# Kernel optimization log

Measured on AMD Instinct MI355X. Metric: run time of the kernel, lower is better.

Reference implementation:

```python
import jax, jax.numpy as jnp
import numpy as np
import math

NB_STEPS = 50  # matches init kwarg nb_steps


def cc_quadrature(nb_steps):
    # Clenshaw-Curtis weights/nodes, identical to UMNN's compute_cc_weights.
    lam = np.arange(nb_steps + 1, dtype=np.float64).reshape(-1, 1)
    lam = np.cos((lam @ lam.T) * math.pi / nb_steps)
    lam[:, 0] = 0.5
    lam[:, -1] = 0.5 * lam[:, -1]
    lam = lam * 2.0 / nb_steps
    W = np.arange(nb_steps + 1, dtype=np.float64).reshape(-1, 1)
    W[np.arange(1, nb_steps + 1, 2)] = 0
    W = 2.0 / (1.0 - W ** 2)
    W[0] = 1
    W[np.arange(1, nb_steps + 1, 2)] = 0
    cc_weights = (lam.T @ W).astype(np.float32)                 # [K, 1]
    steps = np.cos(np.arange(nb_steps + 1, dtype=np.float64).reshape(-1, 1)
                   * math.pi / nb_steps).astype(np.float32)     # [K, 1]
    return jnp.asarray(cc_weights), jnp.asarray(steps)


def integrand_mlp(xh, W1, b1, W2, b2, W3, b3, W4, b4):
    y = jax.nn.relu(jnp.einsum('bkd,hd->bkh', xh, W1) + b1)
    y = jax.nn.relu(jnp.einsum('bkh,gh->bkg', y, W2) + b2)
    y = jax.nn.relu(jnp.einsum('bkg,fg->bkf', y, W3) + b3)
    y = jnp.einsum('bkf,of->bko', y, W4) + b4
    return jax.nn.elu(y) + 1.0


def setup_inputs() -> dict:
    key = jax.random.key(0)
    ks = jax.random.split(key, 10)
    B, HD, IN_D = 16384, 128, 64
    x = jax.random.normal(ks[0], (B, 1), dtype=jnp.float32)
    h = jax.random.normal(ks[1], (B, IN_D - 1), dtype=jnp.float32)
    def lin(k, fan_out, fan_in):
        return jax.random.normal(k, (fan_out, fan_in), dtype=jnp.float32) / np.sqrt(fan_in)
    return {
        'x': x, 'h': h,
        'W1': lin(ks[2], HD, IN_D), 'b1': jax.random.normal(ks[3], (HD,), dtype=jnp.float32) * 0.01,
        'W2': lin(ks[4], HD, HD),   'b2': jax.random.normal(ks[5], (HD,), dtype=jnp.float32) * 0.01,
        'W3': lin(ks[6], HD, HD),   'b3': jax.random.normal(ks[7], (HD,), dtype=jnp.float32) * 0.01,
        'W4': lin(ks[8], 1, HD),    'b4': jax.random.normal(ks[9], (1,), dtype=jnp.float32) * 0.01,
    }


def reference(x, h, W1, b1, W2, b2, W3, b3, W4, b4):
    cc_w, steps = cc_quadrature(NB_STEPS)          # [K,1], [K,1]
    xmax = jnp.max(x) + 10.0
    x0 = x                                          # [B,1]
    xT = jnp.zeros_like(x) + xmax                   # xfinal broadcast
    # quadrature points X_steps: [B, K, 1]
    X = x0[:, None, :] + (xT - x0)[:, None, :] * (steps[None, :, :] + 1.0) * 0.5
    B, K = X.shape[0], X.shape[1]
    hK = jnp.broadcast_to(h[:, None, :], (B, K, h.shape[1]))
    xh = jnp.concatenate([X, hK], axis=-1)          # [B, K, in_d]
    f = integrand_mlp(xh, W1, b1, W2, b2, W3, b3, W4, b4)  # [B, K, 1]
    z = jnp.sum(f * cc_w[None, :, :], axis=1)       # [B, 1]
    return z * (xT - x0) * 0.5
```

## Files before the change

kernel.cpp:

```cpp
#include <hip/hip_runtime.h>
#include <hip/hip_bf16.h>
#include <math.h>


#define B_N    16384
#define KQ     51
#define HD     128
#define IND    64
#define BLK    128
#define RPB    16
#define GRID   (B_N / RPB)
#define TPB    ((RPB * KQ) / 16)

typedef __attribute__((ext_vector_type(8))) short short8;
typedef __attribute__((ext_vector_type(4))) float f32x4;

union S8U { short8 s8; unsigned u[4]; };

__device__ __forceinline__ unsigned short f2bf(float f) {
    __hip_bfloat16 t = __float2bfloat16(f);
    return *reinterpret_cast<unsigned short*>(&t);
}

#if defined(__gfx950__) && defined(__has_builtin)
#if __has_builtin(__builtin_amdgcn_cvt_pk_bf16_f32)
#define HAVE_PK_BF16 1
#endif
#endif

__device__ __forceinline__ unsigned pk_bf16(float lo, float hi) {
#ifdef HAVE_PK_BF16
    typedef __attribute__((ext_vector_type(2))) __bf16 bfv2;
    bfv2 r = __builtin_amdgcn_cvt_pk_bf16_f32(lo, hi);
    return *reinterpret_cast<unsigned*>(&r);
#else
    return (unsigned)f2bf(lo) | ((unsigned)f2bf(hi) << 16);
#endif
}

__launch_bounds__(BLK, 2)
__global__ void umnn_fused(const float* __restrict__ x,  const float* __restrict__ h,
                           const float* __restrict__ W1, const float* __restrict__ b1,
                           const float* __restrict__ W2, const float* __restrict__ b2,
                           const float* __restrict__ W3, const float* __restrict__ b3,
                           const float* __restrict__ W4, const float* __restrict__ b4,
                           float* __restrict__ out)
{
    __shared__ __align__(16) float hpL[RPB * HD];
    __shared__ __align__(16) char  y2x[2][4096];
    __shared__ __align__(16) float hshT[63 * 20];
    __shared__ __align__(16) float vs4[TPB * 64];
    __shared__ __align__(16) float b2f[HD], b3f[HD];
    __shared__ float xL[RPB];
    __shared__ float sSteps[KQ], sCcw[KQ];
    __shared__ float red2[2];

    const int tid  = threadIdx.x;
    const int w    = tid >> 6;
    const int lane = tid & 63;
    const int q    = lane >> 4;
    const int lm   = lane & 15;
    const int swz  = lm & 7;
    const int rowBase = blockIdx.x * RPB;

    if (tid < KQ) {
        const int j = tid;
        const float pi50 = 0.06283185307179586f;
        sSteps[j] = __cosf((float)j * pi50);
        float s = 0.0f;
        for (int i = 0; i <= 50; i += 2) {
            float Wi = (i == 0) ? 1.0f : 2.0f / (1.0f - (float)(i * i));
            float lam;
            if (j == 0) lam = 0.5f;
            else {
                int mp = (i * j) % 100;
                lam = __cosf((float)mp * pi50);
                if (j == 50) lam *= 0.5f;
            }
            s += (lam * 0.04f) * Wi;
        }
        sCcw[j] = s;
    }
    if (tid < HD) {
        b2f[tid] = b2[tid];
        b3f[tid] = b3[tid];
    }
    {
        const f32x4* x4 = (const f32x4*)x;
        float mx = -1e30f;
        for (int i = tid; i < B_N / 4; i += BLK) {
            f32x4 v = x4[i];
            mx = fmaxf(fmaxf(mx, fmaxf(v[0], v[1])), fmaxf(v[2], v[3]));
        }
        #pragma unroll
        for (int d = 32; d > 0; d >>= 1) mx = fmaxf(mx, __shfl_xor(mx, d));
        if (lane == 0) red2[w] = mx;
    }
    for (int i = tid; i < RPB * 63; i += BLK) {
        int r = i / 63, d = i - r * 63;
        hshT[d * 20 + r] = h[rowBase * 63 + i];
    }
    if (tid < RPB) xL[tid] = x[rowBase + tid];
    __syncthreads();

    const float xmax = fmaxf(red2[0], red2[1]) + 10.0f;

    {
        const int n = tid;
        float acc[RPB];
        const float b1v = b1[n];
        #pragma unroll
        for (int r = 0; r < RPB; ++r) acc[r] = b1v;
        const float* wr = W1 + n * IND + 1;
        #pragma unroll 1
        for (int d = 0; d < IND - 1; ++d) {
            float wv = wr[d];
            const float* ht = hshT + d * 20;
            #pragma unroll
            for (int rc = 0; rc < RPB / 4; ++rc) {
                f32x4 hv = *(const f32x4*)(ht + rc * 4);
                acc[rc * 4 + 0] = fmaf(wv, hv[0], acc[rc * 4 + 0]);
                acc[rc * 4 + 1] = fmaf(wv, hv[1], acc[rc * 4 + 1]);
                acc[rc * 4 + 2] = fmaf(wv, hv[2], acc[rc * 4 + 2]);
                acc[rc * 4 + 3] = fmaf(wv, hv[3], acc[rc * 4 + 3]);
            }
        }
        #pragma unroll
        for (int r = 0; r < RPB; ++r) hpL[r * HD + n] = acc[r];
    }
    __syncthreads();

    const int bIoff = q * 16;

    if (w == 0) {
        __builtin_amdgcn_s_setprio(0);
        float w1x[32];
        #pragma unroll
        for (int kk = 0; kk < 4; ++kk)
            #pragma unroll
            for (int j = 0; j < 8; ++j)
                w1x[kk * 8 + j] = W1[(kk * 32 + q * 8 + j) * IND];

        short8 W2A[8][4];
        #pragma unroll
        for (int nt = 0; nt < 8; ++nt) {
            #pragma unroll
            for (int kk = 0; kk < 4; ++kk) {
                const float* p2 = W2 + (nt * 16 + lm) * HD + kk * 32 + q * 8;
                S8U a2;
                #pragma unroll
                for (int j = 0; j < 4; ++j)
                    a2.u[j] = pk_bf16(p2[2 * j], p2[2 * j + 1]);
                W2A[nt][kk] = a2.s8;
            }
        }
        int wrOff[8];
        #pragma unroll
        for (int nt = 0; nt < 8; ++nt)
            wrOff[nt] = lm * 256 + (((2 * nt + (q >> 1)) ^ swz) << 4) + ((q & 1) << 3);
        const char* b2c = (const char*)b2f;

        #pragma unroll 1
        for (int tt = 0; tt < TPB; ++tt) {
            const int s    = tt * 16 + lm;
            const unsigned row = (unsigned)s / KQ;
            const int k    = s - (int)row * KQ;
            const float x0 = xL[row];
            const float X  = fmaf((xmax - x0) * 0.5f, sSteps[k] + 1.0f, x0);
            short8 Y1[4];
            #pragma unroll
            for (int kk = 0; kk < 4; ++kk) {
                const float* hp = hpL + row * HD + kk * 32 + q * 8;
                f32x4 ha = *(const f32x4*)hp;
                f32x4 hb = *(const f32x4*)(hp + 4);
                S8U u;
                u.u[0] = pk_bf16(fmaxf(fmaf(X, w1x[kk*8+0], ha[0]), 0.f),
                                 fmaxf(fmaf(X, w1x[kk*8+1], ha[1]), 0.f));
                u.u[1] = pk_bf16(fmaxf(fmaf(X, w1x[kk*8+2], ha[2]), 0.f),
                                 fmaxf(fmaf(X, w1x[kk*8+3], ha[3]), 0.f));
                u.u[2] = pk_bf16(fmaxf(fmaf(X, w1x[kk*8+4], hb[0]), 0.f),
                                 fmaxf(fmaf(X, w1x[kk*8+5], hb[1]), 0.f));
                u.u[3] = pk_bf16(fmaxf(fmaf(X, w1x[kk*8+6], hb[2]), 0.f),
                                 fmaxf(fmaf(X, w1x[kk*8+7], hb[3]), 0.f));
                Y1[kk] = u.s8;
            }

            f32x4 C[8];
            #pragma unroll
            for (int nt = 0; nt < 8; ++nt)
                C[nt] = *(const f32x4*)(b2c + nt * 64 + bIoff);
            #pragma unroll
            for (int kk = 0; kk < 4; ++kk)
                #pragma unroll
                for (int nt = 0; nt < 8; ++nt)
                    C[nt] = __builtin_amdgcn_mfma_f32_16x16x32_bf16(W2A[nt][kk], Y1[kk], C[nt], 0, 0, 0);

            char* d2 = y2x[tt & 1];
            #pragma unroll
            for (int nt = 0; nt < 8; ++nt) {
                unsigned lo = pk_bf16(fmaxf(C[nt][0], 0.f), fmaxf(C[nt][1], 0.f));
                unsigned hi = pk_bf16(fmaxf(C[nt][2], 0.f), fmaxf(C[nt][3], 0.f));
                *(int2*)(d2 + wrOff[nt]) = make_int2((int)lo, (int)hi);
            }
            __syncthreads();
        }
    } else {
        __builtin_amdgcn_s_setprio(1);
        short8 W3A[8][4];
        f32x4  W4c[8];
        #pragma unroll
        for (int nt = 0; nt < 8; ++nt) {
            #pragma unroll
            for (int kk = 0; kk < 4; ++kk) {
                const float* p3 = W3 + (nt * 16 + lm) * HD + kk * 32 + q * 8;
                S8U a3;
                #pragma unroll
                for (int j = 0; j < 4; ++j)
                    a3.u[j] = pk_bf16(p3[2 * j], p3[2 * j + 1]);
                W3A[nt][kk] = a3.s8;
            }
            W4c[nt] = *(const f32x4*)(W4 + nt * 16 + q * 4);
        }
        const float b4v = b4[0];
        int rdOff[4];
        #pragma unroll
        for (int kk = 0; kk < 4; ++kk)
            rdOff[kk] = lm * 256 + (((kk * 4 + q) ^ swz) << 4);
        const char* b3c = (const char*)b3f;

        #pragma unroll 1
        for (int tt = 0; tt < TPB; ++tt) {
            __syncthreads();
            const char* s2 = y2x[tt & 1];

            short8 Y2[4];
            #pragma unroll
            for (int kk = 0; kk < 4; ++kk)
                Y2[kk] = *(const short8*)(s2 + rdOff[kk]);
            f32x4 C[8];
            #pragma unroll
            for (int nt = 0; nt < 8; ++nt)
                C[nt] = *(const f32x4*)(b3c + nt * 64 + bIoff);

            #pragma unroll
            for (int kk = 0; kk < 4; ++kk)
                #pragma unroll
                for (int nt = 0; nt < 8; ++nt)
                    C[nt] = __builtin_amdgcn_mfma_f32_16x16x32_bf16(W3A[nt][kk], Y2[kk], C[nt], 0, 0, 0);

            float p = 0.f;
            #pragma unroll
            for (int nt = 0; nt < 8; ++nt) {
                p = fmaf(fmaxf(C[nt][0], 0.f), W4c[nt][0], p);
                p = fmaf(fmaxf(C[nt][1], 0.f), W4c[nt][1], p);
                p = fmaf(fmaxf(C[nt][2], 0.f), W4c[nt][2], p);
                p = fmaf(fmaxf(C[nt][3], 0.f), W4c[nt][3], p);
            }
            vs4[tt * 64 + lane] = p;
        }

        {
            const int r   = lane >> 2;
            const int sub = lane & 3;
            float a = 0.f;
            #pragma unroll 1
            for (int j = 0; j < 13; ++j) {
                int k = sub + 4 * j;
                if (k < KQ) {
                    int s   = r * KQ + k;
                    int tt  = s >> 4;
                    int lm2 = s & 15;
                    const float* vb = vs4 + tt * 64 + lm2;
                    float y4 = vb[0] + vb[16] + vb[32] + vb[48] + b4v;
                    float f  = (y4 > 0.f) ? (y4 + 1.f) : __expf(y4);
                    a = fmaf(f, sCcw[k], a);
                }
            }
            a += __shfl_xor(a, 1);
            a += __shfl_xor(a, 2);
            if (sub == 0)
                out[rowBase + r] = a * (xmax - xL[r]) * 0.5f;
        }
    }
}

extern "C" void kernel_launch(void* const* d_in, const int* in_sizes, int n_in,
                              void* d_out, int out_size, void* d_ws, size_t ws_size,
                              hipStream_t stream)
{
    const float* x  = (const float*)d_in[0];
    const float* h  = (const float*)d_in[1];
    const float* W1 = (const float*)d_in[2];
    const float* b1 = (const float*)d_in[3];
    const float* W2 = (const float*)d_in[4];
    const float* b2 = (const float*)d_in[5];
    const float* W3 = (const float*)d_in[6];
    const float* b3 = (const float*)d_in[7];
    const float* W4 = (const float*)d_in[8];
    const float* b4 = (const float*)d_in[9];
    float* out = (float*)d_out;

    umnn_fused<<<GRID, BLK, 0, stream>>>(x, h, W1, b1, W2, b2, W3, b3,
                                         W4, b4, out);
}
```

Measured before the change: 170.1 us.

## Compute first layer with bf16 MFMA per tile instead of FP32 h-projection prologue

Drops the scalar FP32 prologue that precomputed W1·h per row, plus the per-tile VALU FMA step that added X·W1[:,0]. Layer 1 now runs as bf16 MFMA inside the producer wave's tile loop. W1 is converted to bf16 in swizzled LDS, h is stored as bf16 with X spliced into column 0, and the result goes through an LDS round trip to reach layer-2 operand layout. The consumer wave also pre-reduces its partial W4 dot products with a cross-lane shuffle, which halves the vs staging buffer. The cost is 16 extra MFMAs per tile on the already-loaded producer wave, and lower precision from rounding X and h to bf16.

```diff
diff --git a/kernel.cpp b/kernel.cpp
--- a/kernel.cpp
+++ b/kernel.cpp
@@ -46,11 +46,12 @@
                            const float* __restrict__ W4, const float* __restrict__ b4,
                            float* __restrict__ out)
 {
-    __shared__ __align__(16) float hpL[RPB * HD];
+    __shared__ __align__(16) char  w1t[HD * 128];
+    __shared__ __align__(16) char  hbf[RPB * 128];
+    __shared__ __align__(16) char  y1s[4096];
     __shared__ __align__(16) char  y2x[2][4096];
-    __shared__ __align__(16) float hshT[63 * 20];
-    __shared__ __align__(16) float vs4[TPB * 64];
-    __shared__ __align__(16) float b2f[HD], b3f[HD];
+    __shared__ __align__(16) float vs2[TPB * 32];
+    __shared__ __align__(16) float b1f[HD], b2f[HD], b3f[HD];
     __shared__ float xL[RPB];
     __shared__ float sSteps[KQ], sCcw[KQ];
     __shared__ float red2[2];
@@ -82,6 +83,7 @@
         sCcw[j] = s;
     }
     if (tid < HD) {
+        b1f[tid] = b1[tid];
         b2f[tid] = b2[tid];
         b3f[tid] = b3[tid];
     }
@@ -96,51 +98,39 @@
         for (int d = 32; d > 0; d >>= 1) mx = fmaxf(mx, __shfl_xor(mx, d));
         if (lane == 0) red2[w] = mx;
     }
-    for (int i = tid; i < RPB * 63; i += BLK) {
-        int r = i / 63, d = i - r * 63;
-        hshT[d * 20 + r] = h[rowBase * 63 + i];
+    {
+        unsigned short* hb = (unsigned short*)hbf;
+        for (int i = tid; i < RPB * 63; i += BLK) {
+            int r = i / 63, d = i - r * 63;
+            hb[r * 64 + d + 1] = f2bf(h[rowBase * 63 + i]);
+        }
+    }
+    {
+        const int n = tid;
+        const float* wr = W1 + n * IND;
+        #pragma unroll
+        for (int sl = 0; sl < 8; ++sl) {
+            int4 v;
+            v.x = (int)pk_bf16(wr[sl * 8 + 0], wr[sl * 8 + 1]);
+            v.y = (int)pk_bf16(wr[sl * 8 + 2], wr[sl * 8 + 3]);
+            v.z = (int)pk_bf16(wr[sl * 8 + 4], wr[sl * 8 + 5]);
+            v.w = (int)pk_bf16(wr[sl * 8 + 6], wr[sl * 8 + 7]);
+            *(int4*)(w1t + n * 128 + ((sl ^ (n & 7)) << 4)) = v;
+        }
     }
     if (tid < RPB) xL[tid] = x[rowBase + tid];
     __syncthreads();
 
     const float xmax = fmaxf(red2[0], red2[1]) + 10.0f;
 
-    {
-        const int n = tid;
-        float acc[RPB];
-        const float b1v = b1[n];
-        #pragma unroll
-        for (int r = 0; r < RPB; ++r) acc[r] = b1v;
-        const float* wr = W1 + n * IND + 1;
-        #pragma unroll 1
-        for (int d = 0; d < IND - 1; ++d) {
-            float wv = wr[d];
-            const float* ht = hshT + d * 20;
-            #pragma unroll
-            for (int rc = 0; rc < RPB / 4; ++rc) {
-                f32x4 hv = *(const f32x4*)(ht + rc * 4);
-                acc[rc * 4 + 0] = fmaf(wv, hv[0], acc[rc * 4 + 0]);
-                acc[rc * 4 + 1] = fmaf(wv, hv[1], acc[rc * 4 + 1]);
-                acc[rc * 4 + 2] = fmaf(wv, hv[2], acc[rc * 4 + 2]);
-                acc[rc * 4 + 3] = fmaf(wv, hv[3], acc[rc * 4 + 3]);
-            }
-        }
-        #pragma unroll
-        for (int r = 0; r < RPB; ++r) hpL[r * HD + n] = acc[r];
-    }
-    __syncthreads();
-
     const int bIoff = q * 16;
+    int rdOff[4];
+    #pragma unroll
+    for (int kk = 0; kk < 4; ++kk)
+        rdOff[kk] = lm * 256 + (((kk * 4 + q) ^ swz) << 4);
 
     if (w == 0) {
         __builtin_amdgcn_s_setprio(0);
-        float w1x[32];
-        #pragma unroll
-        for (int kk = 0; kk < 4; ++kk)
-            #pragma unroll
-            for (int j = 0; j < 8; ++j)
-                w1x[kk * 8 + j] = W1[(kk * 32 + q * 8 + j) * IND];
-
         short8 W2A[8][4];
         #pragma unroll
         for (int nt = 0; nt < 8; ++nt) {
@@ -158,7 +148,13 @@
         #pragma unroll
         for (int nt = 0; nt < 8; ++nt)
             wrOff[nt] = lm * 256 + (((2 * nt + (q >> 1)) ^ swz) << 4) + ((q & 1) << 3);
+        int rdW1[2];
+        #pragma unroll
+        for (int kk = 0; kk < 2; ++kk)
+            rdW1[kk] = lm * 128 + (((kk * 4 + q) ^ swz) << 4);
+        const char* b1c = (const char*)b1f;
         const char* b2c = (const char*)b2f;
+        const int hOff = q * 16;
 
         #pragma unroll 1
         for (int tt = 0; tt < TPB; ++tt) {
@@ -167,25 +163,41 @@
             const int k    = s - (int)row * KQ;
             const float x0 = xL[row];
             const float X  = fmaf((xmax - x0) * 0.5f, sSteps[k] + 1.0f, x0);
+            const unsigned xb = (unsigned)f2bf(X);
+
+            short8 XH[2];
+            #pragma unroll
+            for (int kk = 0; kk < 2; ++kk)
+                XH[kk] = *(const short8*)(hbf + row * 128 + kk * 64 + hOff);
+            {
+                S8U u; u.s8 = XH[0];
+                u.u[0] = (q == 0) ? ((u.u[0] & 0xffff0000u) | xb) : u.u[0];
+                XH[0] = u.s8;
+            }
+
+            f32x4 C[8];
+            #pragma unroll
+            for (int nt = 0; nt < 8; ++nt)
+                C[nt] = *(const f32x4*)(b1c + nt * 64 + bIoff);
+            #pragma unroll
+            for (int kk = 0; kk < 2; ++kk)
+                #pragma unroll
+                for (int nt = 0; nt < 8; ++nt) {
+                    short8 W1f = *(const short8*)(w1t + nt * 2048 + rdW1[kk]);
+                    C[nt] = __builtin_amdgcn_mfma_f32_16x16x32_bf16(W1f, XH[kk], C[nt], 0, 0, 0);
+                }
+
+            #pragma unroll
+            for (int nt = 0; nt < 8; ++nt) {
+                unsigned lo = pk_bf16(fmaxf(C[nt][0], 0.f), fmaxf(C[nt][1], 0.f));
+                unsigned hi = pk_bf16(fmaxf(C[nt][2], 0.f), fmaxf(C[nt][3], 0.f));
+                *(int2*)(y1s + wrOff[nt]) = make_int2((int)lo, (int)hi);
+            }
             short8 Y1[4];
             #pragma unroll
-            for (int kk = 0; kk < 4; ++kk) {
-                const float* hp = hpL + row * HD + kk * 32 + q * 8;
-                f32x4 ha = *(const f32x4*)hp;
-                f32x4 hb = *(const f32x4*)(hp + 4);
-                S8U u;
-                u.u[0] = pk_bf16(fmaxf(fmaf(X, w1x[kk*8+0], ha[0]), 0.f),
-                                 fmaxf(fmaf(X, w1x[kk*8+1], ha[1]), 0.f));
-                u.u[1] = pk_bf16(fmaxf(fmaf(X, w1x[kk*8+2], ha[2]), 0.f),
-                                 fmaxf(fmaf(X, w1x[kk*8+3], ha[3]), 0.f));
-                u.u[2] = pk_bf16(fmaxf(fmaf(X, w1x[kk*8+4], hb[0]), 0.f),
-                                 fmaxf(fmaf(X, w1x[kk*8+5], hb[1]), 0.f));
-                u.u[3] = pk_bf16(fmaxf(fmaf(X, w1x[kk*8+6], hb[2]), 0.f),
-                                 fmaxf(fmaf(X, w1x[kk*8+7], hb[3]), 0.f));
-                Y1[kk] = u.s8;
-            }
-
-            f32x4 C[8];
+            for (int kk = 0; kk < 4; ++kk)
+                Y1[kk] = *(const short8*)(y1s + rdOff[kk]);
+
             #pragma unroll
             for (int nt = 0; nt < 8; ++nt)
                 C[nt] = *(const f32x4*)(b2c + nt * 64 + bIoff);
@@ -222,10 +234,6 @@
             W4c[nt] = *(const f32x4*)(W4 + nt * 16 + q * 4);
         }
         const float b4v = b4[0];
-        int rdOff[4];
-        #pragma unroll
-        for (int kk = 0; kk < 4; ++kk)
-            rdOff[kk] = lm * 256 + (((kk * 4 + q) ^ swz) << 4);
         const char* b3c = (const char*)b3f;
 
         #pragma unroll 1
@@ -256,7 +264,8 @@
                 p = fmaf(fmaxf(C[nt][2], 0.f), W4c[nt][2], p);
                 p = fmaf(fmaxf(C[nt][3], 0.f), W4c[nt][3], p);
             }
-            vs4[tt * 64 + lane] = p;
+            p += __shfl_xor(p, 32);
+            if (lane < 32) vs2[tt * 32 + lane] = p;
         }
 
         {
@@ -270,8 +279,7 @@
                     int s   = r * KQ + k;
                     int tt  = s >> 4;
                     int lm2 = s & 15;
-                    const float* vb = vs4 + tt * 64 + lm2;
-                    float y4 = vb[0] + vb[16] + vb[32] + vb[48] + b4v;
+                    float y4 = vs2[tt * 32 + lm2] + vs2[tt * 32 + 16 + lm2] + b4v;
                     float f  = (y4 > 0.f) ? (y4 + 1.f) : __expf(y4);
                     a = fmaf(f, sCcw[k], a);
                 }
```

Measured after the change: 175.7 us. 3.3% more time.
